# Kernel optimization log

Hardware: AMD Instinct MI355X
Metric: run time of the kernel (lower is better)

Reference implementation:

```python
import jax, jax.numpy as jnp
import numpy as np

B, S, E, H = 2, 2048, 1024, 16
D = E // H  # head dim = 64
MAX_REL = 512


def setup_inputs() -> dict:
    key = jax.random.key(0)
    ks = jax.random.split(key, 12)
    w = 1.0 / np.sqrt(E)
    return {
        "query": jax.random.normal(ks[0], (B, S, E), jnp.float32),
        "key": jax.random.normal(ks[1], (B, S, E), jnp.float32),
        "value": jax.random.normal(ks[2], (B, S, E), jnp.float32),
        "Wq": jax.random.normal(ks[3], (E, E), jnp.float32) * w,
        "bq": jax.random.normal(ks[4], (E,), jnp.float32) * 0.02,
        "Wk": jax.random.normal(ks[5], (E, E), jnp.float32) * w,
        "bk": jax.random.normal(ks[6], (E,), jnp.float32) * 0.02,
        "Wv": jax.random.normal(ks[7], (E, E), jnp.float32) * w,
        "bv": jax.random.normal(ks[8], (E,), jnp.float32) * 0.02,
        "Wo": jax.random.normal(ks[9], (E, E), jnp.float32) * w,
        "bo": jax.random.normal(ks[10], (E,), jnp.float32) * 0.02,
        "rel_bias_table": jax.random.normal(ks[11], (2 * MAX_REL + 1, H), jnp.float32),
    }


def _rel_bias(rel_bias_table, sq, sk):
    # clamped relative positions -> [Sq, Sk] indices into table
    rel = jnp.arange(sq)[:, None] - jnp.arange(sk)[None, :]
    rel = jnp.clip(rel, -MAX_REL, MAX_REL) + MAX_REL
    bias = rel_bias_table[rel]                 # [Sq, Sk, H]
    return jnp.transpose(bias, (2, 0, 1))[None]  # [1, H, Sq, Sk]


def reference(query, key, value, Wq, bq, Wk, bk, Wv, bv, Wo, bo, rel_bias_table):
    b, sq, e = query.shape
    sk = key.shape[1]
    scale = D ** -0.5
    # projections (torch Linear: x @ W.T + b), split heads -> [B, H, S, D]
    q = (query @ Wq.T + bq).reshape(b, sq, H, D).transpose(0, 2, 1, 3)
    k = (key @ Wk.T + bk).reshape(b, sk, H, D).transpose(0, 2, 1, 3)
    v = (value @ Wv.T + bv).reshape(b, sk, H, D).transpose(0, 2, 1, 3)
    scores = jnp.einsum("bhqd,bhkd->bhqk", q, k) * scale
    scores = scores + _rel_bias(rel_bias_table, sq, sk)
    # causal mask (causal_mask=True branch)
    causal = jnp.arange(sk)[None, :] > jnp.arange(sq)[:, None]
    scores = jnp.where(causal[None, None], -jnp.inf, scores)
    attn = jax.nn.softmax(scores, axis=-1)
    out = jnp.einsum("bhqk,bhkd->bhqd", attn, v)
    out = out.transpose(0, 2, 1, 3).reshape(b, sq, e)
    out = out @ Wo.T + bo
    return out, attn
```

## Files before the change

kernel.cpp:

```cpp
#include <hip/hip_runtime.h>
#include <hip/hip_bf16.h>
#include <stdint.h>

#define Sx 2048
#define Ex 1024
#define Hx 16
#define Dx 64

typedef __attribute__((ext_vector_type(8))) short short8;
typedef __attribute__((ext_vector_type(4))) short bh4;
typedef __attribute__((ext_vector_type(4))) float f32x4;
typedef __attribute__((ext_vector_type(2))) unsigned int u32x2;

__device__ inline short f2bf(float f) {
    unsigned u = __builtin_bit_cast(unsigned, f);
    u = (u + 0x7fffu + ((u >> 16) & 1u)) >> 16;
    return (short)u;
}

__device__ inline unsigned cvtpk_bf16(float a, float b) {
    unsigned r;
    asm("v_cvt_pk_bf16_f32 %0, %1, %2" : "=v"(r) : "v"(a), "v"(b));
    return r;
}

__device__ inline float exp2fast(float x) { return __builtin_amdgcn_exp2f(x); }

__device__ inline void gload16(const short* g, short* l) {
    __builtin_amdgcn_global_load_lds((const __attribute__((address_space(1))) void*)g,
                                     (__attribute__((address_space(3))) void*)l, 16, 0, 0);
}

__global__ __launch_bounds__(256) void prep(const float* __restrict__ q,
                                            const float* __restrict__ k,
                                            const float* __restrict__ v,
                                            const float* __restrict__ wq,
                                            const float* __restrict__ wk,
                                            const float* __restrict__ wv_,
                                            const float* __restrict__ wo,
                                            short* __restrict__ ws) {
    const int seg = blockIdx.y;
    const float* src; size_t n, doff;
    switch (seg) {
        case 0: src = q;   n = 4194304; doff = 0;        break;
        case 1: src = k;   n = 4194304; doff = 4194304;  break;
        case 2: src = v;   n = 4194304; doff = 8388608;  break;
        case 3: src = wq;  n = 1048576; doff = 12582912; break;
        case 4: src = wk;  n = 1048576; doff = 13631488; break;
        case 5: src = wv_; n = 1048576; doff = 14680064; break;
        default: src = wo; n = 1048576; doff = 15728640; break;
    }
    short* dst = ws + doff;
    for (size_t i = ((size_t)blockIdx.x * 256 + threadIdx.x) * 8; i < n;
         i += (size_t)gridDim.x * 256 * 8) {
        float4 f0 = *(const float4*)&src[i];
        float4 f1 = *(const float4*)&src[i + 4];
        short8 s;
        s[0]=f2bf(f0.x); s[1]=f2bf(f0.y); s[2]=f2bf(f0.z); s[3]=f2bf(f0.w);
        s[4]=f2bf(f1.x); s[5]=f2bf(f1.y); s[6]=f2bf(f1.z); s[7]=f2bf(f1.w);
        *(short8*)&dst[i] = s;
    }
}

__global__ __launch_bounds__(256) void gemm_qkv3(const short* __restrict__ wsb,
                                                 const float* __restrict__ bq,
                                                 const float* __restrict__ bk,
                                                 const float* __restrict__ bv,
                                                 short* __restrict__ qh,
                                                 short* __restrict__ kh,
                                                 short* __restrict__ vt) {
    __shared__ short wt[128 * 64];
    __shared__ short xt[128 * 64];
    const int z = blockIdx.z;
    const short* X  = wsb + (size_t)z * 4194304;
    const short* Wm = wsb + 12582912 + (size_t)z * 1048576;
    const float* bias = (z == 0) ? bq : (z == 1) ? bk : bv;
    short* outb = (z == 0) ? qh : (z == 1) ? kh : vt;
    const bool vmode = (z == 2);

    const int tid = threadIdx.x;
    const int l = tid & 63, wv = tid >> 6;
    const int r15 = l & 15, g = l >> 4;
    const int wm = wv >> 1, wn = wv & 1;
    const int i0 = blockIdx.x << 7;
    const int j0 = blockIdx.y << 7;
    const int lrow = l >> 3, lgi = l & 7;

    f32x4 acc[4][4] = {};

    for (int k0 = 0; k0 < Ex; k0 += 64) {
        __syncthreads();
        #pragma unroll
        for (int p = 0; p < 4; ++p) {
            int row = p * 32 + wv * 8 + lrow;
            int col = ((lgi ^ (row & 7)) << 3) + k0;
            gload16(&Wm[(size_t)(j0 + row) * Ex + col], &wt[(p * 32 + wv * 8) * 64]);
            gload16(&X [(size_t)(i0 + row) * Ex + col], &xt[(p * 32 + wv * 8) * 64]);
        }
        __syncthreads();
        const short* At = vmode ? xt : wt;
        const short* Bt = vmode ? wt : xt;
        #pragma unroll
        for (int kk = 0; kk < 64; kk += 32) {
            const int sw = (((kk >> 3) + g) ^ (r15 & 7)) << 3;
            short8 a[4], b[4];
            #pragma unroll
            for (int m = 0; m < 4; ++m)
                a[m] = *(const short8*)&At[(wm * 64 + m * 16 + r15) * 64 + sw];
            #pragma unroll
            for (int n = 0; n < 4; ++n)
                b[n] = *(const short8*)&Bt[(wn * 64 + n * 16 + r15) * 64 + sw];
            #pragma unroll
            for (int m = 0; m < 4; ++m)
                #pragma unroll
                for (int n = 0; n < 4; ++n)
                    acc[m][n] = __builtin_amdgcn_mfma_f32_16x16x32_bf16(a[m], b[n], acc[m][n], 0, 0, 0);
        }
    }

    if (!vmode) {
        #pragma unroll
        for (int m = 0; m < 4; ++m) {
            int jb = j0 + wm * 64 + m * 16 + (g << 2);
            float4 bvv = *(const float4*)&bias[jb];
            #pragma unroll
            for (int n = 0; n < 4; ++n) {
                int i = i0 + wn * 64 + n * 16 + r15;
                bh4 s;
                s[0] = f2bf(acc[m][n][0] + bvv.x);
                s[1] = f2bf(acc[m][n][1] + bvv.y);
                s[2] = f2bf(acc[m][n][2] + bvv.z);
                s[3] = f2bf(acc[m][n][3] + bvv.w);
                *(bh4*)&outb[(size_t)i * Ex + jb] = s;
            }
        }
    } else {
        #pragma unroll
        for (int m = 0; m < 4; ++m) {
            int ib = i0 + wm * 64 + m * 16 + (g << 2);
            int b_ = ib >> 11, s0 = ib & 2047;
            #pragma unroll
            for (int n = 0; n < 4; ++n) {
                int j = j0 + wn * 64 + n * 16 + r15;
                float bj = bias[j];
                bh4 s;
                s[0] = f2bf(acc[m][n][0] + bj);
                s[1] = f2bf(acc[m][n][1] + bj);
                s[2] = f2bf(acc[m][n][2] + bj);
                s[3] = f2bf(acc[m][n][3] + bj);
                *(bh4*)&outb[((size_t)(b_ * Hx + (j >> 6)) * Dx + (j & 63)) * Sx + s0] = s;
            }
        }
    }
}

__global__ __launch_bounds__(256) void gemm_out(const short* __restrict__ Xb,
                                                const short* __restrict__ Wb,
                                                const float* __restrict__ bias,
                                                float* __restrict__ out) {
    __shared__ short wt[2][128 * 64];
    __shared__ short xt[2][128 * 64];
    const int tid = threadIdx.x;
    const int l = tid & 63, wv = tid >> 6;
    const int r15 = l & 15, g = l >> 4;
    const int wm = wv >> 1, wn = wv & 1;
    const int i0 = blockIdx.x << 7;
    const int j0 = blockIdx.y << 7;
    const int lrow = l >> 3, lgi = l & 7;

    f32x4 acc[4][4] = {};

    auto stage = [&](int it, int buf) {
        int k0 = it << 6;
        #pragma unroll
        for (int p = 0; p < 4; ++p) {
            int row = p * 32 + wv * 8 + lrow;
            int col = ((lgi ^ (row & 7)) << 3) + k0;
            gload16(&Wb[(size_t)(j0 + row) * Ex + col], &wt[buf][(p * 32 + wv * 8) * 64]);
            gload16(&Xb[(size_t)(i0 + row) * Ex + col], &xt[buf][(p * 32 + wv * 8) * 64]);
        }
    };

    stage(0, 0);
    for (int it = 0; it < 16; ++it) {
        __syncthreads();
        if (it + 1 < 16) stage(it + 1, (it + 1) & 1);
        const int cur = it & 1;
        #pragma unroll
        for (int kk = 0; kk < 64; kk += 32) {
            const int sw = (((kk >> 3) + g) ^ (r15 & 7)) << 3;
            short8 a[4], b[4];
            #pragma unroll
            for (int m = 0; m < 4; ++m)
                a[m] = *(const short8*)&wt[cur][(wm * 64 + m * 16 + r15) * 64 + sw];
            #pragma unroll
            for (int n = 0; n < 4; ++n)
                b[n] = *(const short8*)&xt[cur][(wn * 64 + n * 16 + r15) * 64 + sw];
            #pragma unroll
            for (int m = 0; m < 4; ++m)
                #pragma unroll
                for (int n = 0; n < 4; ++n)
                    acc[m][n] = __builtin_amdgcn_mfma_f32_16x16x32_bf16(a[m], b[n], acc[m][n], 0, 0, 0);
        }
    }

    #pragma unroll
    for (int m = 0; m < 4; ++m) {
        int jb = j0 + wm * 64 + m * 16 + (g << 2);
        float4 bvv = *(const float4*)&bias[jb];
        #pragma unroll
        for (int n = 0; n < 4; ++n) {
            int i = i0 + wn * 64 + n * 16 + r15;
            float4 o;
            o.x = acc[m][n][0] + bvv.x;
            o.y = acc[m][n][1] + bvv.y;
            o.z = acc[m][n][2] + bvv.z;
            o.w = acc[m][n][3] + bvv.w;
            *(float4*)&out[(size_t)i * Ex + jb] = o;
        }
    }
}

__global__ __launch_bounds__(256) void attn_fused(const short* __restrict__ qhat,
                                                  const short* __restrict__ khat,
                                                  const short* __restrict__ vT,
                                                  const float* __restrict__ table,
                                                  float* __restrict__ attn,
                                                  short* __restrict__ om) {
    __shared__ short qs[128 * 64];
    __shared__ short ks[2][64 * 64];
    __shared__ short vs[2][64 * 64];
    __shared__ short ps[128 * 64];
    __shared__ float bl[1028];

    const int tid = threadIdx.x;
    const int l = tid & 63, wv = tid >> 6;
    const int r15 = l & 15, g = l >> 4;

    const int lin = blockIdx.x + (blockIdx.y << 4);
    const int xcd = lin & 7, slot = lin >> 3;
    const int bh = xcd + ((slot & 3) << 3);
    const int qidx = (slot >> 2) & 7;
    const int qt = (slot >> 5) ? (15 - qidx) : qidx;

    const int b = bh >> 4, h = bh & 15;
    const int lrow = l >> 3, lgi = l & 7;
    const int nkt = 2 * qt + 2;
    const float cs2 = 0.18033688f;

    for (int i = tid; i < 1025; i += 256)
        bl[i] = (i < 512) ? -3e30f : (table[i * Hx + h] - 16.0f) * 1.4426950408889634f;

    #pragma unroll
    for (int p = 0; p < 4; ++p) {
        int row = p * 32 + wv * 8 + lrow;
        gload16(&qhat[(size_t)(b * Sx + (qt << 7) + row) * Ex + h * Dx + ((lgi ^ (row & 7)) << 3)],
                &qs[(p * 32 + wv * 8) * 64]);
    }

    auto stageK = [&](int kt, int buf) {
        #pragma unroll
        for (int p = 0; p < 2; ++p) {
            int row = p * 32 + wv * 8 + lrow;
            gload16(&khat[(size_t)(b * Sx + (kt << 6) + row) * Ex + h * Dx + ((lgi ^ (row & 7)) << 3)],
                    &ks[buf][(p * 32 + wv * 8) * 64]);
        }
    };
    auto stageV = [&](int kt, int buf) {
        #pragma unroll
        for (int p = 0; p < 2; ++p) {
            int row = p * 32 + wv * 8 + lrow;
            gload16(&vT[((size_t)bh * Dx + row) * Sx + (kt << 6) + ((lgi ^ (row & 7)) << 3)],
                    &vs[buf][(p * 32 + wv * 8) * 64]);
        }
    };

    float sr[2] = {0.f, 0.f};
    const int qg0 = (qt << 7) + wv * 32 + r15;

    stageK(0, 0);
    for (int kt = 0; kt < nkt; ++kt) {
        __syncthreads();
        if (kt + 1 < nkt) stageK(kt + 1, (kt + 1) & 1);
        const int cur = kt & 1;
        f32x4 sf[4][2] = {};
        __builtin_amdgcn_s_setprio(1);
        #pragma unroll
        for (int kk = 0; kk < 64; kk += 32) {
            const int sw = (((kk >> 3) + g) ^ (r15 & 7)) << 3;
            short8 a[4], bq[2];
            #pragma unroll
            for (int m = 0; m < 4; ++m) a[m] = *(const short8*)&ks[cur][(m * 16 + r15) * 64 + sw];
            #pragma unroll
            for (int n = 0; n < 2; ++n) bq[n] = *(const short8*)&qs[(wv * 32 + n * 16 + r15) * 64 + sw];
            #pragma unroll
            for (int m = 0; m < 4; ++m)
                #pragma unroll
                for (int n = 0; n < 2; ++n)
                    sf[m][n] = __builtin_amdgcn_mfma_f32_16x16x32_bf16(a[m], bq[n], sf[m][n], 0, 0, 0);
        }
        __builtin_amdgcn_s_setprio(0);
        const int kcb = (kt << 6) + (g << 2);
        #pragma unroll
        for (int n = 0; n < 2; ++n) {
            int base = qg0 + n * 16 + 512 - kcb;
            float psum = 0.f;
            #pragma unroll
            for (int m = 0; m < 4; ++m) {
                int b0 = base - m * 16;
                #pragma unroll
                for (int r = 0; r < 4; ++r) {
                    int idx = b0 - r;
                    idx = idx > 1024 ? 1024 : idx;
                    psum += exp2fast(fmaf(sf[m][n][r], cs2, bl[idx]));
                }
            }
            psum += __shfl_xor(psum, 16);
            psum += __shfl_xor(psum, 32);
            sr[n] += psum;
        }
    }

    float inv[2] = {1.0f / sr[0], 1.0f / sr[1]};
    f32x4 of[4][2] = {};
    float* Ap = attn + (size_t)bh * ((size_t)Sx * Sx);

    __syncthreads();
    stageK(0, 0);
    stageV(0, 0);
    for (int kt = 0; kt < nkt; ++kt) {
        __syncthreads();
        if (kt + 1 < nkt) { stageK(kt + 1, (kt + 1) & 1); stageV(kt + 1, (kt + 1) & 1); }
        const int cur = kt & 1;
        f32x4 sf[4][2] = {};
        __builtin_amdgcn_s_setprio(1);
        #pragma unroll
        for (int kk = 0; kk < 64; kk += 32) {
            const int sw = (((kk >> 3) + g) ^ (r15 & 7)) << 3;
            short8 a[4], bq[2];
            #pragma unroll
            for (int m = 0; m < 4; ++m) a[m] = *(const short8*)&ks[cur][(m * 16 + r15) * 64 + sw];
            #pragma unroll
            for (int n = 0; n < 2; ++n) bq[n] = *(const short8*)&qs[(wv * 32 + n * 16 + r15) * 64 + sw];
            #pragma unroll
            for (int m = 0; m < 4; ++m)
                #pragma unroll
                for (int n = 0; n < 2; ++n)
                    sf[m][n] = __builtin_amdgcn_mfma_f32_16x16x32_bf16(a[m], bq[n], sf[m][n], 0, 0, 0);
        }
        __builtin_amdgcn_s_setprio(0);
        #pragma unroll
        for (int n = 0; n < 2; ++n) {
            int q = qg0 + n * 16;
            int qrow = wv * 32 + n * 16 + r15;
            #pragma unroll
            for (int m = 0; m < 4; ++m) {
                int kc0 = (kt << 6) + m * 16 + (g << 2);
                int b0 = q + 512 - kc0;
                f32x4 pv;
                #pragma unroll
                for (int r = 0; r < 4; ++r) {
                    int idx = b0 - r;
                    idx = idx > 1024 ? 1024 : idx;
                    pv[r] = exp2fast(fmaf(sf[m][n][r], cs2, bl[idx])) * inv[n];
                }
                __builtin_nontemporal_store(pv, (f32x4*)&Ap[(size_t)q * Sx + kc0]);
                u32x2 pk;
                pk[0] = cvtpk_bf16(pv[0], pv[1]);
                pk[1] = cvtpk_bf16(pv[2], pv[3]);
                int gphys = (m * 2 + (g >> 1)) ^ (r15 & 7);
                *(u32x2*)&ps[qrow * 64 + gphys * 8 + (g & 1) * 4] = pk;
            }
        }
        __builtin_amdgcn_s_setprio(1);
        #pragma unroll
        for (int kk = 0; kk < 64; kk += 32) {
            const int sw = (((kk >> 3) + g) ^ (r15 & 7)) << 3;
            short8 a[4], bp[2];
            #pragma unroll
            for (int m = 0; m < 4; ++m) a[m] = *(const short8*)&vs[cur][(m * 16 + r15) * 64 + sw];
            #pragma unroll
            for (int n = 0; n < 2; ++n) bp[n] = *(const short8*)&ps[(wv * 32 + n * 16 + r15) * 64 + sw];
            #pragma unroll
            for (int m = 0; m < 4; ++m)
                #pragma unroll
                for (int n = 0; n < 2; ++n)
                    of[m][n] = __builtin_amdgcn_mfma_f32_16x16x32_bf16(a[m], bp[n], of[m][n], 0, 0, 0);
        }
        __builtin_amdgcn_s_setprio(0);
    }

    #pragma unroll
    for (int m = 0; m < 4; ++m) {
        int d0 = m * 16 + (g << 2);
        #pragma unroll
        for (int n = 0; n < 2; ++n) {
            int qv = (qt << 7) + wv * 32 + n * 16 + r15;
            u32x2 s;
            s[0] = cvtpk_bf16(of[m][n][0], of[m][n][1]);
            s[1] = cvtpk_bf16(of[m][n][2], of[m][n][3]);
            *(u32x2*)&om[(size_t)(b * Sx + qv) * Ex + h * Dx + d0] = s;
        }
    }

    const int c0 = nkt << 6;
    f32x4 z = {0.f, 0.f, 0.f, 0.f};
    for (int row = tid >> 3; row < 128; row += 32) {
        size_t base = (size_t)((qt << 7) + row) * Sx;
        for (int c = c0 + ((tid & 7) << 2); c < Sx; c += 32)
            __builtin_nontemporal_store(z, (f32x4*)&Ap[base + c]);
    }
}

extern "C" void kernel_launch(void* const* d_in, const int* in_sizes, int n_in,
                              void* d_out, int out_size, void* d_ws, size_t ws_size,
                              hipStream_t stream) {
    const float* query = (const float*)d_in[0];
    const float* key   = (const float*)d_in[1];
    const float* value = (const float*)d_in[2];
    const float* bq = (const float*)d_in[4];
    const float* bk = (const float*)d_in[6];
    const float* bv = (const float*)d_in[8];
    const float* bo = (const float*)d_in[10];
    const float* Wq = (const float*)d_in[3];
    const float* Wk = (const float*)d_in[5];
    const float* Wv = (const float*)d_in[7];
    const float* Wo = (const float*)d_in[9];
    const float* tbl = (const float*)d_in[11];

    short* ws = (short*)d_ws;
    short* qx  = ws;
    short* wob = ws + 15728640;
    short* qh  = ws + 16777216;
    short* kh  = ws + 20971520;
    short* vt  = ws + 25165824;

    float* outp  = (float*)d_out;
    float* attnp = outp + 4194304;

    prep<<<dim3(1024, 7), 256, 0, stream>>>(query, key, value, Wq, Wk, Wv, Wo, ws);
    gemm_qkv3<<<dim3(32, 8, 3), 256, 0, stream>>>(ws, bq, bk, bv, qh, kh, vt);
    attn_fused<<<dim3(16, 32), 256, 0, stream>>>(qh, kh, vt, tbl, attnp, qx);
    gemm_out<<<dim3(32, 8), 256, 0, stream>>>(qx, wob, bo, outp);
}
```

Before: 274.9 us.

## Use 8 waves per attention block with Q fragments held in registers

The attention kernel now runs 512 threads per block, so each of 8 waves owns 16 query rows instead of 4 waves owning 32. The Q tile is loaded straight from global memory into register fragments rather than staged through shared memory. K/V staging and zero-filling are spread across the larger thread count. This raises wave-level parallelism and frees shared memory, but removes the per-wave reuse of K fragments across two query subtiles, so LDS reads of K/V per MFMA double, and launch_bounds was removed.

```diff
diff --git a/kernel.cpp b/kernel.cpp
--- a/kernel.cpp
+++ b/kernel.cpp
@@ -221,13 +221,12 @@
     }
 }
 
-__global__ __launch_bounds__(256) void attn_fused(const short* __restrict__ qhat,
-                                                  const short* __restrict__ khat,
-                                                  const short* __restrict__ vT,
-                                                  const float* __restrict__ table,
-                                                  float* __restrict__ attn,
-                                                  short* __restrict__ om) {
-    __shared__ short qs[128 * 64];
+__global__ void attn_fused(const short* __restrict__ qhat,
+                           const short* __restrict__ khat,
+                           const short* __restrict__ vT,
+                           const float* __restrict__ table,
+                           float* __restrict__ attn,
+                           short* __restrict__ om) {
     __shared__ short ks[2][64 * 64];
     __shared__ short vs[2][64 * 64];
     __shared__ short ps[128 * 64];
@@ -248,81 +247,69 @@
     const int nkt = 2 * qt + 2;
     const float cs2 = 0.18033688f;
 
-    for (int i = tid; i < 1025; i += 256)
+    for (int i = tid; i < 1025; i += 512)
         bl[i] = (i < 512) ? -3e30f : (table[i * Hx + h] - 16.0f) * 1.4426950408889634f;
 
-    #pragma unroll
-    for (int p = 0; p < 4; ++p) {
-        int row = p * 32 + wv * 8 + lrow;
-        gload16(&qhat[(size_t)(b * Sx + (qt << 7) + row) * Ex + h * Dx + ((lgi ^ (row & 7)) << 3)],
-                &qs[(p * 32 + wv * 8) * 64]);
+    short8 qf[2];
+    {
+        const size_t qrow = (size_t)(b * Sx + (qt << 7) + wv * 16 + r15);
+        #pragma unroll
+        for (int kk = 0; kk < 2; ++kk)
+            qf[kk] = *(const short8*)&qhat[qrow * Ex + h * Dx + kk * 32 + g * 8];
     }
 
     auto stageK = [&](int kt, int buf) {
-        #pragma unroll
-        for (int p = 0; p < 2; ++p) {
-            int row = p * 32 + wv * 8 + lrow;
-            gload16(&khat[(size_t)(b * Sx + (kt << 6) + row) * Ex + h * Dx + ((lgi ^ (row & 7)) << 3)],
-                    &ks[buf][(p * 32 + wv * 8) * 64]);
-        }
+        int row = wv * 8 + lrow;
+        gload16(&khat[(size_t)(b * Sx + (kt << 6) + row) * Ex + h * Dx + ((lgi ^ (row & 7)) << 3)],
+                &ks[buf][(wv * 8) * 64]);
     };
     auto stageV = [&](int kt, int buf) {
-        #pragma unroll
-        for (int p = 0; p < 2; ++p) {
-            int row = p * 32 + wv * 8 + lrow;
-            gload16(&vT[((size_t)bh * Dx + row) * Sx + (kt << 6) + ((lgi ^ (row & 7)) << 3)],
-                    &vs[buf][(p * 32 + wv * 8) * 64]);
-        }
+        int row = wv * 8 + lrow;
+        gload16(&vT[((size_t)bh * Dx + row) * Sx + (kt << 6) + ((lgi ^ (row & 7)) << 3)],
+                &vs[buf][(wv * 8) * 64]);
     };
 
-    float sr[2] = {0.f, 0.f};
-    const int qg0 = (qt << 7) + wv * 32 + r15;
+    float sr = 0.f;
+    const int qg0 = (qt << 7) + wv * 16 + r15;
 
     stageK(0, 0);
     for (int kt = 0; kt < nkt; ++kt) {
         __syncthreads();
         if (kt + 1 < nkt) stageK(kt + 1, (kt + 1) & 1);
         const int cur = kt & 1;
-        f32x4 sf[4][2] = {};
+        f32x4 sf[4] = {};
         __builtin_amdgcn_s_setprio(1);
         #pragma unroll
         for (int kk = 0; kk < 64; kk += 32) {
             const int sw = (((kk >> 3) + g) ^ (r15 & 7)) << 3;
-            short8 a[4], bq[2];
+            short8 a[4];
             #pragma unroll
             for (int m = 0; m < 4; ++m) a[m] = *(const short8*)&ks[cur][(m * 16 + r15) * 64 + sw];
             #pragma unroll
-            for (int n = 0; n < 2; ++n) bq[n] = *(const short8*)&qs[(wv * 32 + n * 16 + r15) * 64 + sw];
-            #pragma unroll
-            for (int m = 0; m < 4; ++m)
-                #pragma unroll
-                for (int n = 0; n < 2; ++n)
-                    sf[m][n] = __builtin_amdgcn_mfma_f32_16x16x32_bf16(a[m], bq[n], sf[m][n], 0, 0, 0);
+            for (int m = 0; m < 4; ++m)
+                sf[m] = __builtin_amdgcn_mfma_f32_16x16x32_bf16(a[m], qf[kk >> 5], sf[m], 0, 0, 0);
         }
         __builtin_amdgcn_s_setprio(0);
         const int kcb = (kt << 6) + (g << 2);
-        #pragma unroll
-        for (int n = 0; n < 2; ++n) {
-            int base = qg0 + n * 16 + 512 - kcb;
-            float psum = 0.f;
-            #pragma unroll
-            for (int m = 0; m < 4; ++m) {
-                int b0 = base - m * 16;
-                #pragma unroll
-                for (int r = 0; r < 4; ++r) {
-                    int idx = b0 - r;
-                    idx = idx > 1024 ? 1024 : idx;
-                    psum += exp2fast(fmaf(sf[m][n][r], cs2, bl[idx]));
-                }
+        int base = qg0 + 512 - kcb;
+        float psum = 0.f;
+        #pragma unroll
+        for (int m = 0; m < 4; ++m) {
+            int b0 = base - m * 16;
+            #pragma unroll
+            for (int r = 0; r < 4; ++r) {
+                int idx = b0 - r;
+                idx = idx > 1024 ? 1024 : idx;
+                psum += exp2fast(fmaf(sf[m][r], cs2, bl[idx]));
             }
-            psum += __shfl_xor(psum, 16);
-            psum += __shfl_xor(psum, 32);
-            sr[n] += psum;
-        }
-    }
-
-    float inv[2] = {1.0f / sr[0], 1.0f / sr[1]};
-    f32x4 of[4][2] = {};
+        }
+        psum += __shfl_xor(psum, 16);
+        psum += __shfl_xor(psum, 32);
+        sr += psum;
+    }
+
+    const float inv = 1.0f / sr;
+    f32x4 of[4] = {};
     float* Ap = attn + (size_t)bh * ((size_t)Sx * Sx);
 
     __syncthreads();
@@ -332,27 +319,22 @@
         __syncthreads();
         if (kt + 1 < nkt) { stageK(kt + 1, (kt + 1) & 1); stageV(kt + 1, (kt + 1) & 1); }
         const int cur = kt & 1;
-        f32x4 sf[4][2] = {};
+        f32x4 sf[4] = {};
         __builtin_amdgcn_s_setprio(1);
         #pragma unroll
         for (int kk = 0; kk < 64; kk += 32) {
             const int sw = (((kk >> 3) + g) ^ (r15 & 7)) << 3;
-            short8 a[4], bq[2];
+            short8 a[4];
             #pragma unroll
             for (int m = 0; m < 4; ++m) a[m] = *(const short8*)&ks[cur][(m * 16 + r15) * 64 + sw];
             #pragma unroll
-            for (int n = 0; n < 2; ++n) bq[n] = *(const short8*)&qs[(wv * 32 + n * 16 + r15) * 64 + sw];
-            #pragma unroll
-            for (int m = 0; m < 4; ++m)
-                #pragma unroll
-                for (int n = 0; n < 2; ++n)
-                    sf[m][n] = __builtin_amdgcn_mfma_f32_16x16x32_bf16(a[m], bq[n], sf[m][n], 0, 0, 0);
+            for (int m = 0; m < 4; ++m)
+                sf[m] = __builtin_amdgcn_mfma_f32_16x16x32_bf16(a[m], qf[kk >> 5], sf[m], 0, 0, 0);
         }
         __builtin_amdgcn_s_setprio(0);
-        #pragma unroll
-        for (int n = 0; n < 2; ++n) {
-            int q = qg0 + n * 16;
-            int qrow = wv * 32 + n * 16 + r15;
+        {
+            const int q = qg0;
+            const int qrow = wv * 16 + r15;
             #pragma unroll
             for (int m = 0; m < 4; ++m) {
                 int kc0 = (kt << 6) + m * 16 + (g << 2);
@@ -362,7 +344,7 @@
                 for (int r = 0; r < 4; ++r) {
                     int idx = b0 - r;
                     idx = idx > 1024 ? 1024 : idx;
-                    pv[r] = exp2fast(fmaf(sf[m][n][r], cs2, bl[idx])) * inv[n];
+                    pv[r] = exp2fast(fmaf(sf[m][r], cs2, bl[idx])) * inv;
                 }
                 __builtin_nontemporal_store(pv, (f32x4*)&Ap[(size_t)q * Sx + kc0]);
                 u32x2 pk;
@@ -376,36 +358,32 @@
         #pragma unroll
         for (int kk = 0; kk < 64; kk += 32) {
             const int sw = (((kk >> 3) + g) ^ (r15 & 7)) << 3;
-            short8 a[4], bp[2];
+            short8 a[4], bp;
             #pragma unroll
             for (int m = 0; m < 4; ++m) a[m] = *(const short8*)&vs[cur][(m * 16 + r15) * 64 + sw];
-            #pragma unroll
-            for (int n = 0; n < 2; ++n) bp[n] = *(const short8*)&ps[(wv * 32 + n * 16 + r15) * 64 + sw];
-            #pragma unroll
-            for (int m = 0; m < 4; ++m)
-                #pragma unroll
-                for (int n = 0; n < 2; ++n)
-                    of[m][n] = __builtin_amdgcn_mfma_f32_16x16x32_bf16(a[m], bp[n], of[m][n], 0, 0, 0);
+            bp = *(const short8*)&ps[(wv * 16 + r15) * 64 + sw];
+            #pragma unroll
+            for (int m = 0; m < 4; ++m)
+                of[m] = __builtin_amdgcn_mfma_f32_16x16x32_bf16(a[m], bp, of[m], 0, 0, 0);
         }
         __builtin_amdgcn_s_setprio(0);
     }
 
-    #pragma unroll
-    for (int m = 0; m < 4; ++m) {
-        int d0 = m * 16 + (g << 2);
-        #pragma unroll
-        for (int n = 0; n < 2; ++n) {
-            int qv = (qt << 7) + wv * 32 + n * 16 + r15;
+    {
+        const int qv = (qt << 7) + wv * 16 + r15;
+        #pragma unroll
+        for (int m = 0; m < 4; ++m) {
+            int d0 = m * 16 + (g << 2);
             u32x2 s;
-            s[0] = cvtpk_bf16(of[m][n][0], of[m][n][1]);
-            s[1] = cvtpk_bf16(of[m][n][2], of[m][n][3]);
+            s[0] = cvtpk_bf16(of[m][0], of[m][1]);
+            s[1] = cvtpk_bf16(of[m][2], of[m][3]);
             *(u32x2*)&om[(size_t)(b * Sx + qv) * Ex + h * Dx + d0] = s;
         }
     }
 
     const int c0 = nkt << 6;
     f32x4 z = {0.f, 0.f, 0.f, 0.f};
-    for (int row = tid >> 3; row < 128; row += 32) {
+    for (int row = tid >> 3; row < 128; row += 64) {
         size_t base = (size_t)((qt << 7) + row) * Sx;
         for (int c = c0 + ((tid & 7) << 2); c < Sx; c += 32)
             __builtin_nontemporal_store(z, (f32x4*)&Ap[base + c]);
@@ -440,6 +418,6 @@
 
     prep<<<dim3(1024, 7), 256, 0, stream>>>(query, key, value, Wq, Wk, Wv, Wo, ws);
     gemm_qkv3<<<dim3(32, 8, 3), 256, 0, stream>>>(ws, bq, bk, bv, qh, kh, vt);
-    attn_fused<<<dim3(16, 32), 256, 0, stream>>>(qh, kh, vt, tbl, attnp, qx);
+    attn_fused<<<dim3(16, 32), 512, 0, stream>>>(qh, kh, vt, tbl, attnp, qx);
     gemm_out<<<dim3(32, 8), 256, 0, stream>>>(qx, wob, bo, outp);
 }
```

Result: no change. 273.7 us (-0.5%).
